# Optimization experiments

Hardware: AMD Instinct MI355X
Metric: run time of the kernel (lower is better)

The kernel has to match this reference:

```python
import jax, jax.numpy as jnp
import numpy as np

SEQ, BATCH, IN, HID, OUT = 512, 64, 512, 1024, 512
KEEP = 0.7  # dropout p = 0.3


def setup_inputs() -> dict:
    key = jax.random.key(0)
    ks = jax.random.split(key, 9)
    def lin(k, fan_out, fan_in):
        bound = 1.0 / np.sqrt(fan_in)
        kw, kb = jax.random.split(k)
        W = jax.random.uniform(kw, (fan_out, fan_in), jnp.float32, -bound, bound)
        b = jax.random.uniform(kb, (fan_out,), jnp.float32, -bound, bound)
        return W, b
    x = jax.random.normal(ks[0], (SEQ, BATCH, IN), jnp.float32)
    # inverted dropout mask, fixed for determinism
    drop_mask = (jax.random.bernoulli(ks[1], KEEP, (SEQ, BATCH, OUT))
                 .astype(jnp.float32) / KEEP)
    W_i2h, b_i2h = lin(ks[2], HID, IN + HID)
    W_i2o, b_i2o = lin(ks[3], OUT, IN + HID)
    W_o2o, b_o2o = lin(ks[4], OUT, HID + OUT)
    return {"x": x, "drop_mask": drop_mask,
            "W_i2h": W_i2h, "b_i2h": b_i2h,
            "W_i2o": W_i2o, "b_i2o": b_i2o,
            "W_o2o": W_o2o, "b_o2o": b_o2o}


def reference(x, drop_mask, W_i2h, b_i2h, W_i2o, b_i2o, W_o2o, b_o2o):
    # x: [S, B, IN]; returns log-probs [S, B, OUT]
    def step(h, inp):
        x_t, m_t = inp  # [B, IN], [B, OUT]
        comb = jnp.concatenate([x_t, h], axis=1)          # [B, IN+HID]
        out = comb @ W_i2o.T + b_i2o                      # [B, OUT]
        h_new = comb @ W_i2h.T + b_i2h                    # [B, HID]
        oc = jnp.concatenate([out, h_new], axis=1) @ W_o2o.T + b_o2o  # [B, OUT]
        oc = oc * m_t                                     # dropout (inverted mask)
        oc = jax.nn.log_softmax(oc, axis=-1)
        return h_new, oc
    h0 = jnp.zeros((x.shape[1], W_i2h.shape[0]), x.dtype)
    _, outs = jax.lax.scan(step, h0, (x, drop_mask))
    return outs
```

## Files before the change

kernel.cpp:

```cpp
#include <hip/hip_runtime.h>
#include <stdint.h>


typedef unsigned short ushort_t;
typedef __attribute__((ext_vector_type(8))) __bf16 bf16x8;
typedef __attribute__((ext_vector_type(4))) float f32x4;

__device__ __forceinline__ ushort_t f2bf(float f) {
  union { float f; uint32_t u; } v; v.f = f;
  uint32_t r = v.u + 0x7fffu + ((v.u >> 16) & 1u);
  return (ushort_t)(r >> 16);
}
__device__ __forceinline__ float bf2f(ushort_t b) {
  union { uint32_t u; float f; } v; v.u = ((uint32_t)b) << 16;
  return v.f;
}
__device__ __forceinline__ void gload16(const ushort_t* g, ushort_t* l) {
  __builtin_amdgcn_global_load_lds(
      (const __attribute__((address_space(1))) uint32_t*)g,
      (__attribute__((address_space(3))) uint32_t*)l, 16, 0, 0);
}

__global__ __launch_bounds__(256) void pack_kernel(
    const float* __restrict__ x, const float* __restrict__ mask,
    const float* __restrict__ W_i2h,
    const float* __restrict__ W_i2o, const float* __restrict__ W_o2o,
    const float* __restrict__ b_i2o, const float* __restrict__ b_o2o,
    ushort_t* xB, ushort_t* Wihx, ushort_t* Whh, ushort_t* Wiox,
    ushort_t* Wioh, ushort_t* Wo1, ushort_t* Wo2, float* biasP,
    uint64_t* maskb, uint32_t* harr0) {
  int64_t i = (int64_t)blockIdx.x * blockDim.x + threadIdx.x;
  const int64_t c0 = 16777216, c1 = 17301504, c2 = 18350080, c3 = 18612224,
                c4 = 19136512, c5 = 19398656, c6 = 19922944,
                cB = 19955712,
                cM = 36732928,
                cI = 36765696;
  if (i < c0) { xB[i] = f2bf(x[i]); return; }
  if (i < c1) { int64_t j = i - c0; int r = j >> 9,  c = j & 511;  Wihx[j] = f2bf(W_i2h[(int64_t)r * 1536 + c]); return; }
  if (i < c2) { int64_t j = i - c1; int r = j >> 10, c = j & 1023; Whh[j]  = f2bf(W_i2h[(int64_t)r * 1536 + 512 + c]); return; }
  if (i < c3) { int64_t j = i - c2; int r = j >> 9,  c = j & 511;  Wiox[j] = f2bf(W_i2o[(int64_t)r * 1536 + c]); return; }
  if (i < c4) { int64_t j = i - c3; int r = j >> 10, c = j & 1023; Wioh[j] = f2bf(W_i2o[(int64_t)r * 1536 + 512 + c]); return; }
  if (i < c5) { int64_t j = i - c4; int r = j >> 9,  c = j & 511;  Wo1[j]  = f2bf(W_o2o[(int64_t)r * 1536 + c]); return; }
  if (i < c6) { int64_t j = i - c5; int r = j >> 10, c = j & 1023; Wo2[j]  = f2bf(W_o2o[(int64_t)r * 1536 + 512 + c]); return; }
  if (i < cB) {
    int64_t q = i - c6;
    const int n = (int)(q >> 6), lane = (int)(q & 63);
    const float* wr = W_o2o + (int64_t)n * 1536;
    float s = 0.f;
#pragma unroll
    for (int k = 0; k < 8; ++k) {
      const int m = lane + 64 * k;
      s += wr[m] * b_i2o[m];
    }
#pragma unroll
    for (int off = 32; off; off >>= 1) s += __shfl_xor(s, off, 64);
    if (lane == 0) biasP[n] = s + b_o2o[n];
    return;
  }
  if (i < cM) {
    int64_t j = i - cB;
    float v = mask[j];
    uint64_t bits = __ballot(v != 0.0f);
    if ((j & 63) == 0) maskb[j >> 6] = bits;
    return;
  }
  if (i < cI) {
    harr0[i - cM] = 0;
  }
}

__device__ void usetup_tile(ushort_t* SH,
    const ushort_t* __restrict__ Wo1, const ushort_t* __restrict__ Wiox,
    const ushort_t* __restrict__ Wioh, ushort_t* __restrict__ U1,
    ushort_t* __restrict__ U2, int job) {
  ushort_t* AsF = SH;
  ushort_t* BsF = SH + 4096;
  const ushort_t* Bm; ushort_t* Om; int mt, nt, ldb;
  if (job < 16) { mt = job >> 2; nt = job & 3; Bm = Wiox; Om = U1; ldb = 512; }
  else { job -= 16; mt = job >> 3; nt = job & 7; Bm = Wioh; Om = U2; ldb = 1024; }
  const int m0 = mt * 128, n0 = nt * 128;
  const int tid = threadIdx.x;
  const int w = tid >> 6, l = tid & 63;
  const int quad = l >> 4, l15 = l & 15;
  const int wm = (w & 1) * 64, wn = (w >> 1) * 64;
  const int r0 = tid >> 2, chunk = tid & 3;
  f32x4 acc[4][4] = {};
  for (int k0 = 0; k0 < 512; k0 += 32) {
    __syncthreads();
    gload16(Wo1 + (size_t)(m0 + r0) * 512 + k0 + chunk * 8,      &AsF[tid * 8]);
    gload16(Wo1 + (size_t)(m0 + r0 + 64) * 512 + k0 + chunk * 8, &AsF[2048 + tid * 8]);
#pragma unroll
    for (int rep = 0; rep < 2; ++rep) {
      const int idx = tid + 256 * rep;
      const int kk = idx & 31, n8 = idx >> 5;
      union { uint4 v; ushort_t s[8]; } u;
      u.v = *(const uint4*)(Bm + (size_t)(k0 + kk) * ldb + n0 + n8 * 8);
#pragma unroll
      for (int i = 0; i < 8; ++i) BsF[(n8 * 8 + i) * 32 + kk] = u.s[i];
    }
    __syncthreads();
    bf16x8 af[4], bfr[4];
#pragma unroll
    for (int i = 0; i < 4; ++i) af[i]  = *(const bf16x8*)&AsF[(wm + 16 * i + l15) * 32 + 8 * quad];
#pragma unroll
    for (int j = 0; j < 4; ++j) bfr[j] = *(const bf16x8*)&BsF[(wn + 16 * j + l15) * 32 + 8 * quad];
#pragma unroll
    for (int i = 0; i < 4; ++i)
#pragma unroll
      for (int j = 0; j < 4; ++j)
        acc[i][j] = __builtin_amdgcn_mfma_f32_16x16x32_bf16(af[i], bfr[j], acc[i][j], 0, 0, 0);
  }
#pragma unroll
  for (int i = 0; i < 4; ++i) {
    const int row = m0 + wm + 16 * i + 4 * quad;
#pragma unroll
    for (int j = 0; j < 4; ++j) {
      const int col = n0 + wn + 16 * j + l15;
#pragma unroll
      for (int r = 0; r < 4; ++r)
        Om[(size_t)(row + r) * ldb + col] = f2bf(acc[i][j][r]);
    }
  }
}

__global__ __launch_bounds__(256) void gemm_bt(
    const ushort_t* __restrict__ A1, int lda1, const ushort_t* __restrict__ B1, int K1,
    const float* __restrict__ bias, ushort_t* Cb, int Ntiles,
    const ushort_t* __restrict__ Wo1, const ushort_t* __restrict__ Wiox,
    const ushort_t* __restrict__ Wioh, ushort_t* __restrict__ U1,
    ushort_t* __restrict__ U2) {
  __shared__ __align__(16) ushort_t SH[16384];
  if (blockIdx.x >= 2048) {
    usetup_tile(SH, Wo1, Wiox, Wioh, U1, U2, blockIdx.x - 2048);
    return;
  }
  const int mt = blockIdx.x & 255, nt = blockIdx.x >> 8;
  const int m0 = mt * 128, n0 = nt * 128;
  const int tid = threadIdx.x;
  const int w = tid >> 6, l = tid & 63;
  const int quad = l >> 4, l15 = l & 15;
  const int wm = (w & 1) * 64, wn = (w >> 1) * 64;
  const int r0 = tid >> 2, chunk = tid & 3;
  f32x4 acc[4][4] = {};
  gload16(A1 + (size_t)(m0 + r0) * lda1 + chunk * 8,      &SH[tid * 8]);
  gload16(A1 + (size_t)(m0 + r0 + 64) * lda1 + chunk * 8, &SH[2048 + tid * 8]);
  gload16(B1 + (size_t)(n0 + r0) * K1 + chunk * 8,        &SH[8192 + tid * 8]);
  gload16(B1 + (size_t)(n0 + r0 + 64) * K1 + chunk * 8,   &SH[8192 + 2048 + tid * 8]);
  const int NIT = K1 >> 5;
  for (int it = 0; it < NIT; ++it) {
    const int p = it & 1;
    const int ao = p * 4096, bo = 8192 + p * 4096;
    __syncthreads();
    if (it + 1 < NIT) {
      const int kn = (it + 1) * 32;
      const int an = (p ^ 1) * 4096, bn = 8192 + (p ^ 1) * 4096;
      gload16(A1 + (size_t)(m0 + r0) * lda1 + kn + chunk * 8,      &SH[an + tid * 8]);
      gload16(A1 + (size_t)(m0 + r0 + 64) * lda1 + kn + chunk * 8, &SH[an + 2048 + tid * 8]);
      gload16(B1 + (size_t)(n0 + r0) * K1 + kn + chunk * 8,        &SH[bn + tid * 8]);
      gload16(B1 + (size_t)(n0 + r0 + 64) * K1 + kn + chunk * 8,   &SH[bn + 2048 + tid * 8]);
    }
    bf16x8 af[4], bfr[4];
#pragma unroll
    for (int i = 0; i < 4; ++i) af[i]  = *(const bf16x8*)&SH[ao + (wm + 16 * i + l15) * 32 + 8 * quad];
#pragma unroll
    for (int j = 0; j < 4; ++j) bfr[j] = *(const bf16x8*)&SH[bo + (wn + 16 * j + l15) * 32 + 8 * quad];
#pragma unroll
    for (int i = 0; i < 4; ++i)
#pragma unroll
      for (int j = 0; j < 4; ++j)
        acc[i][j] = __builtin_amdgcn_mfma_f32_16x16x32_bf16(af[i], bfr[j], acc[i][j], 0, 0, 0);
  }
  const int N = Ntiles * 128;
#pragma unroll
  for (int i = 0; i < 4; ++i) {
    const int row = m0 + wm + 16 * i + 4 * quad;
#pragma unroll
    for (int j = 0; j < 4; ++j) {
      const int col = n0 + wn + 16 * j + l15;
      const float bv = bias[col];
#pragma unroll
      for (int r = 0; r < 4; ++r)
        Cb[(size_t)(row + r) * N + col] = f2bf(acc[i][j][r] + bv);
    }
  }
}

template<int NTERMS>
__device__ void pair_tile128T(ushort_t* SH,
    const ushort_t* __restrict__ A0r0, const ushort_t* __restrict__ A0r1,
    const ushort_t* __restrict__ B0,
    const ushort_t* __restrict__ A1r0, const ushort_t* __restrict__ A1r1,
    const ushort_t* __restrict__ B1,
    int n0, const ushort_t* __restrict__ Xh, ushort_t* __restrict__ Oh,
    int gate) {
  const int tid = threadIdx.x;
  const int w = tid >> 6, l = tid & 63;
  const int quad = l >> 4, l15 = l & 15;
  const int wm = (w & 1) * 64, wn = (w >> 1) * 64;
  const int r0 = tid >> 2, chunk = tid & 3;
  const int thrA  = r0 * 1024 + chunk * 8;
  const int thrB0 = (n0 + r0) * 1024 + chunk * 8;
  const int thrB1 = (n0 + r0 + 64) * 1024 + chunk * 8;
  const ushort_t* ga0 = A0r0 + thrA;
  const ushort_t* ga1 = A0r1 + thrA;
  const ushort_t* gb0 = B0 + thrB0;
  const ushort_t* gb1 = B0 + thrB1;
  f32x4 acc[4][4] = {};
  gload16(ga0, &SH[tid * 8]);
  gload16(ga1, &SH[2048 + tid * 8]);
  gload16(gb0, &SH[8192 + tid * 8]);
  gload16(gb1, &SH[8192 + 2048 + tid * 8]);
  const int NIT = NTERMS * 32;
  for (int it = 0; it < NIT; ++it) {
    const int p = it & 1;
    const int ap = p * 4096, bp = 8192 + p * 4096;
    __syncthreads();
    if (it + 1 < NIT) {
      if (NTERMS == 2 && it == 31) {
        ga0 = A1r0 + thrA; ga1 = A1r1 + thrA;
        gb0 = B1 + thrB0;  gb1 = B1 + thrB1;
      } else {
        ga0 += 32; ga1 += 32; gb0 += 32; gb1 += 32;
      }
      const int an = (p ^ 1) * 4096, bn = 8192 + (p ^ 1) * 4096;
      gload16(ga0, &SH[an + tid * 8]);
      gload16(ga1, &SH[an + 2048 + tid * 8]);
      gload16(gb0, &SH[bn + tid * 8]);
      gload16(gb1, &SH[bn + 2048 + tid * 8]);
    }
    bf16x8 af[4], bfr[4];
#pragma unroll
    for (int i = 0; i < 4; ++i) af[i]  = *(const bf16x8*)&SH[ap + (wm + 16 * i + l15) * 32 + 8 * quad];
#pragma unroll
    for (int j = 0; j < 4; ++j) bfr[j] = *(const bf16x8*)&SH[bp + (wn + 16 * j + l15) * 32 + 8 * quad];
#pragma unroll
    for (int i = 0; i < 4; ++i)
#pragma unroll
      for (int j = 0; j < 4; ++j)
        acc[i][j] = __builtin_amdgcn_mfma_f32_16x16x32_bf16(af[i], bfr[j], acc[i][j], 0, 0, 0);
  }
#pragma unroll
  for (int i = 0; i < 4; ++i) {
#pragma unroll
    for (int j = 0; j < 4; ++j) {
      const int col = n0 + wn + 16 * j + l15;
#pragma unroll
      for (int r = 0; r < 4; ++r) {
        const int lrow = 16 * i + 4 * quad + r;
        const size_t idx = (size_t)lrow * 1024 + col;
        float v = gate ? acc[i][j][r] : 0.0f;
        Oh[idx] = f2bf(v + bf2f(Xh[idx]));
      }
    }
  }
}

__device__ void copy_tile(const ushort_t* X, ushort_t* O, int n0) {
  const int t = threadIdx.x, r = t >> 2, q = t & 3;
  const uint4* src = (const uint4*)(X + (size_t)r * 1024 + n0 + q * 32);
  uint4* dst = (uint4*)(O + (size_t)r * 1024 + n0 + q * 32);
  dst[0] = src[0]; dst[1] = src[1]; dst[2] = src[2]; dst[3] = src[3];
}

__device__ void power_tile(ushort_t* SH,
                           const ushort_t* __restrict__ Am,
                           const ushort_t* __restrict__ Bm,
                           ushort_t* __restrict__ Om, int t) {
  ushort_t* AsF = SH;
  ushort_t* BsF = SH + 4096;
  const int mt = t & 7, nt = (t >> 3) & 7;
  const int m0 = mt * 128, n0 = nt * 128;
  const int tid = threadIdx.x;
  const int w = tid >> 6, l = tid & 63;
  const int quad = l >> 4, l15 = l & 15;
  const int wm = (w & 1) * 64, wn = (w >> 1) * 64;
  const int r0 = tid >> 2, chunk = tid & 3;
  f32x4 acc[4][4] = {};
  for (int k0 = 0; k0 < 1024; k0 += 32) {
    __syncthreads();
    gload16(Am + (size_t)(m0 + r0) * 1024 + k0 + chunk * 8,      &AsF[tid * 8]);
    gload16(Am + (size_t)(m0 + r0 + 64) * 1024 + k0 + chunk * 8, &AsF[2048 + tid * 8]);
#pragma unroll
    for (int rep = 0; rep < 2; ++rep) {
      const int idx = tid + 256 * rep;
      const int kk = idx & 31, n8 = idx >> 5;
      union { uint4 v; ushort_t s[8]; } u;
      u.v = *(const uint4*)(Bm + (size_t)(k0 + kk) * 1024 + n0 + n8 * 8);
#pragma unroll
      for (int i = 0; i < 8; ++i) BsF[(n8 * 8 + i) * 32 + kk] = u.s[i];
    }
    __syncthreads();
    bf16x8 af[4], bfr[4];
#pragma unroll
    for (int i = 0; i < 4; ++i) af[i]  = *(const bf16x8*)&AsF[(wm + 16 * i + l15) * 32 + 8 * quad];
#pragma unroll
    for (int j = 0; j < 4; ++j) bfr[j] = *(const bf16x8*)&BsF[(wn + 16 * j + l15) * 32 + 8 * quad];
#pragma unroll
    for (int i = 0; i < 4; ++i)
#pragma unroll
      for (int j = 0; j < 4; ++j)
        acc[i][j] = __builtin_amdgcn_mfma_f32_16x16x32_bf16(af[i], bfr[j], acc[i][j], 0, 0, 0);
  }
#pragma unroll
  for (int i = 0; i < 4; ++i) {
    const int row = m0 + wm + 16 * i + 4 * quad;
#pragma unroll
    for (int j = 0; j < 4; ++j) {
      const int col = n0 + wn + 16 * j + l15;
#pragma unroll
      for (int r = 0; r < 4; ++r)
        Om[(size_t)(row + r) * 1024 + col] = f2bf(acc[i][j][r]);
    }
  }
}

#define PWp(idx) (Pw + (size_t)(idx) * 1048576)

__global__ __launch_bounds__(256) void pass_kernel(
    const ushort_t* __restrict__ XhB, ushort_t* __restrict__ Harr,
    const ushort_t* __restrict__ Whh, ushort_t* __restrict__ Pw, int mode) {
  __shared__ __align__(16) ushort_t SH[16384];
  const int bid = blockIdx.x;
  const int npow = (mode == 1) ? 64 : ((mode == 2) ? 128 : 256);
  if (bid < npow) {
    const int pj = bid >> 6, t = bid & 63;
    const ushort_t *Am, *Bm; ushort_t* Om;
    if (mode == 1)      { Am = Whh;    Bm = Whh;    Om = PWp(0); }
    else if (mode == 2) {
      if (pj == 0) { Am = Whh;    Bm = PWp(0); Om = PWp(1); }
      else         { Am = PWp(0); Bm = PWp(0); Om = PWp(2); }
    } else {
      switch (pj) {
        case 0:  Am = Whh;    Bm = PWp(2); Om = PWp(3); break;
        case 1:  Am = PWp(0); Bm = PWp(2); Om = PWp(4); break;
        case 2:  Am = PWp(1); Bm = PWp(2); Om = PWp(5); break;
        default: Am = PWp(2); Bm = PWp(2); Om = PWp(6); break;
      }
    }
    power_tile(SH, Am, Bm, Om, t);
    return;
  }
  const int inner0 = bid - npow;
  const int u = inner0 >> 8, inner = inner0 & 255;
  const int p_ = (inner & 7) | (((inner >> 6) & 3) << 3);
  const int n0 = ((inner >> 3) & 7) * 128;
#define HS_(s) (Harr + (size_t)(s) * 65536)
#define XS_(s) (XhB + (size_t)(s) * 65536)
  const ushort_t *A0, *B0, *A1 = nullptr, *B1 = nullptr, *X; ushort_t* O;
  int terms = 1;
  if (mode == 1) {
    const int as[4] = {0, 2, 4, 6}, xs[4] = {1, 3, 5, 7}, os[4] = {2, 4, 1, 8};
    A0 = XS_(as[u]); B0 = Whh; X = XS_(xs[u]); O = HS_(os[u]);
  } else if (mode == 2) {
    if (u == 0)      { A0 = HS_(2); B0 = Whh;    X = XS_(2); O = HS_(3); }
    else if (u == 1) { A0 = HS_(2); B0 = PWp(0); X = HS_(4); O = HS_(4); }
    else             { A0 = HS_(1); B0 = PWp(0); X = HS_(8); O = HS_(8); }
  } else {
    if (u == 0)      { A0 = HS_(4); B0 = Whh;    X = XS_(4); O = HS_(5); }
    else if (u == 1) { A0 = HS_(4); B0 = PWp(0); X = HS_(1); O = HS_(6); }
    else if (u == 2) { A0 = HS_(1); B0 = Whh; A1 = HS_(4); B1 = PWp(1);
                       terms = 2;               X = XS_(6); O = HS_(7); }
    else             { A0 = HS_(4); B0 = PWp(2); X = HS_(8); O = HS_(8); }
  }
  const size_t co0 = (size_t)(2 * p_) * 524288;
  const size_t co1 = co0 + 524288;
  const int half = (threadIdx.x >> 6) & 1;
  const size_t coh = half ? co1 : co0;
  if (terms == 2)
    pair_tile128T<2>(SH, A0 + co0, A0 + co1, B0, A1 + co0, A1 + co1, B1,
                     n0, X + coh, O + coh, 1);
  else
    pair_tile128T<1>(SH, A0 + co0, A0 + co1, B0, nullptr, nullptr, nullptr,
                     n0, X + coh, O + coh, 1);
}

__global__ __launch_bounds__(256) void scan64(
    const ushort_t* __restrict__ old, ushort_t* __restrict__ nw,
    const ushort_t* __restrict__ Pv, int d,
    const ushort_t* __restrict__ Pra, ushort_t* __restrict__ Pwo, int nride) {
  __shared__ __align__(16) ushort_t SH[16384];
  if (blockIdx.x < nride) {
    power_tile(SH, Pra, Pra, Pwo, blockIdx.x);
    return;
  }
  const int bid = blockIdx.x - nride;
  const int p_ = (bid & 7) | (((bid >> 6) & 3) << 3);
  const int n0 = ((bid >> 3) & 7) * 128;
  const int c0 = 2 * p_, c1 = c0 + 1;
  if (c1 < d) {
    copy_tile(old + (size_t)c0 * 524288, nw + (size_t)c0 * 524288, n0);
    copy_tile(old + (size_t)c1 * 524288, nw + (size_t)c1 * 524288, n0);
    return;
  }
  const int ia0 = (c0 >= d) ? (c0 - d) : 0;
  const int ia1 = c1 - d;
  const int half = (threadIdx.x >> 6) & 1;
  const int ch = half ? c1 : c0;
  const int gate = (ch >= d);
  pair_tile128T<1>(SH, old + (size_t)ia0 * 524288, old + (size_t)ia1 * 524288,
                   Pv, nullptr, nullptr, nullptr, n0,
                   old + (size_t)ch * 524288, nw + (size_t)ch * 524288, gate);
}

__global__ __launch_bounds__(256) void correct_kernel(
    const ushort_t* __restrict__ S, const ushort_t* __restrict__ XhB,
    ushort_t* __restrict__ Harr, const ushort_t* __restrict__ Whh,
    const ushort_t* __restrict__ Pw) {
  __shared__ __align__(16) ushort_t AsF[2][4096];
  __shared__ __align__(16) ushort_t BsF[2][4096];
  const int p_ = blockIdx.x >> 3;
  const int n0 = (blockIdx.x & 7) * 128;
  const int j = blockIdx.y + 1;
  const ushort_t* Wj = (j == 1) ? Whh : (Pw + (size_t)(j - 2) * 1048576);
  const ushort_t* Xs = (j == 1) ? XhB : (Harr + (size_t)j * 65536);
  ushort_t* XO = Harr + (size_t)j * 65536;
  const int tid = threadIdx.x;
  const int w = tid >> 6, l = tid & 63;
  const int quad = l >> 4, l15 = l & 15;
  const int wm = (w & 1) * 64, wn = (w >> 1) * 64;
  const int r0 = tid >> 2, chunk = tid & 3;
  f32x4 acc[4][4] = {};
  const ushort_t* a0 = S + (size_t)(2 * p_) * 524288 + (size_t)r0 * 1024;
  const ushort_t* a1 = S + (size_t)(2 * p_ + 1) * 524288 + (size_t)r0 * 1024;
  gload16(a0 + chunk * 8, &AsF[0][tid * 8]);
  gload16(a1 + chunk * 8, &AsF[0][2048 + tid * 8]);
  gload16(Wj + (size_t)(n0 + r0) * 1024 + chunk * 8,      &BsF[0][tid * 8]);
  gload16(Wj + (size_t)(n0 + r0 + 64) * 1024 + chunk * 8, &BsF[0][2048 + tid * 8]);
  for (int it = 0; it < 32; ++it) {
    const int p = it & 1;
    __syncthreads();
    if (it < 31) {
      const int kn = (it + 1) * 32;
      gload16(a0 + kn + chunk * 8, &AsF[p ^ 1][tid * 8]);
      gload16(a1 + kn + chunk * 8, &AsF[p ^ 1][2048 + tid * 8]);
      gload16(Wj + (size_t)(n0 + r0) * 1024 + kn + chunk * 8,      &BsF[p ^ 1][tid * 8]);
      gload16(Wj + (size_t)(n0 + r0 + 64) * 1024 + kn + chunk * 8, &BsF[p ^ 1][2048 + tid * 8]);
    }
    bf16x8 af[4], bfr[4];
#pragma unroll
    for (int i = 0; i < 4; ++i) af[i]  = *(const bf16x8*)&AsF[p][(wm + 16 * i + l15) * 32 + 8 * quad];
#pragma unroll
    for (int jj = 0; jj < 4; ++jj) bfr[jj] = *(const bf16x8*)&BsF[p][(wn + 16 * jj + l15) * 32 + 8 * quad];
#pragma unroll
    for (int i = 0; i < 4; ++i)
#pragma unroll
      for (int jj = 0; jj < 4; ++jj)
        acc[i][jj] = __builtin_amdgcn_mfma_f32_16x16x32_bf16(af[i], bfr[jj], acc[i][jj], 0, 0, 0);
  }
#pragma unroll
  for (int i = 0; i < 4; ++i) {
#pragma unroll
    for (int jj = 0; jj < 4; ++jj) {
      const int col = n0 + wn + 16 * jj + l15;
#pragma unroll
      for (int r = 0; r < 4; ++r) {
        const int gr = wm + 16 * i + 4 * quad + r;
        const int c = 2 * p_ + (gr >> 6);
        const size_t idx = (size_t)c * 524288 + (size_t)(gr & 63) * 1024 + col;
        XO[idx] = f2bf(acc[i][jj][r] + bf2f(Xs[idx]));
      }
    }
  }
}

__global__ __launch_bounds__(256) void gemm_fused(
    const ushort_t* __restrict__ xB, const ushort_t* __restrict__ U1,
    const ushort_t* __restrict__ Harr, const ushort_t* __restrict__ U2,
    const ushort_t* __restrict__ Wo2, const float* __restrict__ biasP,
    const uint64_t* __restrict__ maskb, float* __restrict__ out) {
  __shared__ __align__(16) ushort_t AsF[2][4096];
  __shared__ __align__(16) ushort_t BsF[2][4096];
  const int mt = blockIdx.x & 255, nt = blockIdx.x >> 8;
  const int m0 = mt * 128, n0 = nt * 128;
  const int tid = threadIdx.x;
  const int w = tid >> 6, l = tid & 63;
  const int quad = l >> 4, l15 = l & 15;
  const int wm = (w & 1) * 64, wn = (w >> 1) * 64;
  const int r0 = tid >> 2, chunk = tid & 3;
  f32x4 acc[4][4] = {};
  auto issue = [&](int it, int b) {
    const ushort_t *A, *B; int K, k0;
    if (it < 16)      { A = xB;           B = U1;  K = 512;  k0 = it << 5; }
    else if (it < 48) { A = Harr;         B = U2;  K = 1024; k0 = (it - 16) << 5; }
    else              { A = Harr + 65536; B = Wo2; K = 1024; k0 = (it - 48) << 5; }
    gload16(A + (size_t)(m0 + r0) * K + k0 + chunk * 8,      &AsF[b][tid * 8]);
    gload16(A + (size_t)(m0 + r0 + 64) * K + k0 + chunk * 8, &AsF[b][2048 + tid * 8]);
    gload16(B + (size_t)(n0 + r0) * K + k0 + chunk * 8,      &BsF[b][tid * 8]);
    gload16(B + (size_t)(n0 + r0 + 64) * K + k0 + chunk * 8, &BsF[b][2048 + tid * 8]);
  };
  issue(0, 0);
  for (int it = 0; it < 80; ++it) {
    const int p = it & 1;
    __syncthreads();
    if (it < 79) issue(it + 1, p ^ 1);
    bf16x8 af[4], bfr[4];
#pragma unroll
    for (int i = 0; i < 4; ++i) af[i]  = *(const bf16x8*)&AsF[p][(wm + 16 * i + l15) * 32 + 8 * quad];
#pragma unroll
    for (int j = 0; j < 4; ++j) bfr[j] = *(const bf16x8*)&BsF[p][(wn + 16 * j + l15) * 32 + 8 * quad];
#pragma unroll
    for (int i = 0; i < 4; ++i)
#pragma unroll
      for (int j = 0; j < 4; ++j)
        acc[i][j] = __builtin_amdgcn_mfma_f32_16x16x32_bf16(af[i], bfr[j], acc[i][j], 0, 0, 0);
  }
  const float INV_KEEP = 1.0f / 0.7f;
#pragma unroll
  for (int i = 0; i < 4; ++i) {
    const int row = m0 + wm + 16 * i + 4 * quad;
#pragma unroll
    for (int j = 0; j < 4; ++j) {
      const int col = n0 + wn + 16 * j + l15;
      const float bv = biasP[col];
#pragma unroll
      for (int r = 0; r < 4; ++r) {
        const size_t idx = (size_t)(row + r) * 512 + col;
        const uint64_t bits = maskb[idx >> 6];
        out[idx] = ((bits >> (idx & 63)) & 1) ? (acc[i][j][r] + bv) * INV_KEEP
                                              : 0.0f;
      }
    }
  }
}

__global__ __launch_bounds__(256) void softmax_kernel(float* __restrict__ out) {
  const int row = blockIdx.x;
  const int tid = threadIdx.x;
  const size_t base = (size_t)row * 512;
  __shared__ float sm[4], ss[4];
  const float v0 = out[base + tid];
  const float v1 = out[base + tid + 256];
  float m = fmaxf(v0, v1);
#pragma unroll
  for (int off = 32; off; off >>= 1) m = fmaxf(m, __shfl_xor(m, off, 64));
  const int w = tid >> 6;
  if ((tid & 63) == 0) sm[w] = m;
  __syncthreads();
  m = fmaxf(fmaxf(sm[0], sm[1]), fmaxf(sm[2], sm[3]));
  float s = __expf(v0 - m) + __expf(v1 - m);
#pragma unroll
  for (int off = 32; off; off >>= 1) s += __shfl_xor(s, off, 64);
  if ((tid & 63) == 0) ss[w] = s;
  __syncthreads();
  s = ss[0] + ss[1] + ss[2] + ss[3];
  const float lg = logf(s);
  out[base + tid] = v0 - m - lg;
  out[base + tid + 256] = v1 - m - lg;
}

extern "C" void kernel_launch(void* const* d_in, const int* in_sizes, int n_in,
                              void* d_out, int out_size, void* d_ws, size_t ws_size,
                              hipStream_t stream) {
  const float* x     = (const float*)d_in[0];
  const float* mask  = (const float*)d_in[1];
  const float* W_i2h = (const float*)d_in[2];
  const float* b_i2h = (const float*)d_in[3];
  const float* W_i2o = (const float*)d_in[4];
  const float* b_i2o = (const float*)d_in[5];
  const float* W_o2o = (const float*)d_in[6];
  const float* b_o2o = (const float*)d_in[7];
  float* out = (float*)d_out;

  char* ws = (char*)d_ws;
  const size_t NEED = 207749120;
  if (ws_size < NEED) return;
  ushort_t* xB   = (ushort_t*)(ws + 0);
  ushort_t* XhB  = (ushort_t*)(ws + 33554432);
  ushort_t* SA   = XhB + 65536;
  ushort_t* SB   = XhB + 3 * 65536;
  ushort_t* Harr = (ushort_t*)(ws + 100663296);
  ushort_t* Pw   = (ushort_t*)(ws + 167903232);
  ushort_t* U1   = (ushort_t*)(ws + 193069056);
  ushort_t* U2   = (ushort_t*)(ws + 193593344);
  float* biasP   = (float*)(ws + 194641920);
  uint64_t* maskb = (uint64_t*)(ws + 195000320);
  ushort_t* Wihx = (ushort_t*)(ws + 201457664);
  ushort_t* Whh  = (ushort_t*)(ws + 202506240);
  ushort_t* Wiox = (ushort_t*)(ws + 204603392);
  ushort_t* Wioh = (ushort_t*)(ws + 205127680);
  ushort_t* Wo1  = (ushort_t*)(ws + 206176256);
  ushort_t* Wo2  = (ushort_t*)(ws + 206700544);

  hipLaunchKernelGGL(pack_kernel, dim3(143616), dim3(256), 0, stream,
                     x, mask, W_i2h, W_i2o, W_o2o, b_i2o, b_o2o,
                     xB, Wihx, Whh, Wiox, Wioh, Wo1, Wo2, biasP, maskb,
                     (uint32_t*)Harr);
  hipLaunchKernelGGL(gemm_bt, dim3(2096), dim3(256), 0, stream,
                     xB, 512, Wihx, 512, b_i2h, XhB, 8,
                     Wo1, Wiox, Wioh, U1, U2);
  hipLaunchKernelGGL(pass_kernel, dim3(1088), dim3(256), 0, stream,
                     XhB, Harr, Whh, Pw, 1);
  hipLaunchKernelGGL(pass_kernel, dim3(896), dim3(256), 0, stream,
                     XhB, Harr, Whh, Pw, 2);
  hipLaunchKernelGGL(pass_kernel, dim3(1280), dim3(256), 0, stream,
                     XhB, Harr, Whh, Pw, 3);
  hipLaunchKernelGGL(scan64, dim3(320), dim3(256), 0, stream, Harr, SB, PWp(6),  1, PWp(6),  PWp(7),  64);
  hipLaunchKernelGGL(scan64, dim3(320), dim3(256), 0, stream, SB, SA, PWp(7),  2, PWp(7),  PWp(8),  64);
  hipLaunchKernelGGL(scan64, dim3(320), dim3(256), 0, stream, SA, SB, PWp(8),  4, PWp(8),  PWp(9),  64);
  hipLaunchKernelGGL(scan64, dim3(320), dim3(256), 0, stream, SB, SA, PWp(9),  8, PWp(9),  PWp(10), 64);
  hipLaunchKernelGGL(scan64, dim3(320), dim3(256), 0, stream, SA, SB, PWp(10), 16, PWp(10), PWp(11), 64);
  hipLaunchKernelGGL(scan64, dim3(256), dim3(256), 0, stream, SB, SA, PWp(11), 32, (const ushort_t*)nullptr, (ushort_t*)nullptr, 0);
  hipLaunchKernelGGL(correct_kernel, dim3(dim3(256, 8)), dim3(256), 0, stream,
                     SA, XhB, Harr, Whh, Pw);
  hipLaunchKernelGGL(gemm_fused, dim3(1024), dim3(256), 0, stream,
                     xB, U1, Harr, U2, Wo2, biasP, maskb, out);
  hipLaunchKernelGGL(softmax_kernel, dim3(32768), dim3(256), 0, stream, out);
}
```

Baseline: 1.113 ms.

## Fold correction GEMM tiles into scan passes and use wave-per-row softmax

Correction tiles for chunk pairs whose scan prefix is already final are now computed inside the later scan64 launches as extra blocks, overlapping them with the remaining scan steps. The standalone correct_kernel then handles only the last 16 pairs. Softmax is rewritten so one wavefront owns a row, with vectorized float4 loads and no shared-memory barriers. This adds complexity around which scan buffer holds finalized prefixes at each step, and a wrong pair-to-step mapping would silently produce incorrect values.

```diff
diff --git a/kernel.cpp b/kernel.cpp
--- a/kernel.cpp
+++ b/kernel.cpp
@@ -316,6 +316,64 @@
 
 #define PWp(idx) (Pw + (size_t)(idx) * 1048576)
 
+__device__ void correct_ride(ushort_t* SH,
+    const ushort_t* __restrict__ S, const ushort_t* __restrict__ XhB,
+    ushort_t* __restrict__ Harr, const ushort_t* __restrict__ Whh,
+    const ushort_t* __restrict__ Pw, int p_, int n0, int j) {
+  const ushort_t* Wj = (j == 1) ? Whh : (Pw + (size_t)(j - 2) * 1048576);
+  const ushort_t* Xs = (j == 1) ? XhB : (Harr + (size_t)j * 65536);
+  ushort_t* XO = Harr + (size_t)j * 65536;
+  const int tid = threadIdx.x;
+  const int w = tid >> 6, l = tid & 63;
+  const int quad = l >> 4, l15 = l & 15;
+  const int wm = (w & 1) * 64, wn = (w >> 1) * 64;
+  const int r0 = tid >> 2, chunk = tid & 3;
+  f32x4 acc[4][4] = {};
+  const ushort_t* a0 = S + (size_t)(2 * p_) * 524288 + (size_t)r0 * 1024;
+  const ushort_t* a1 = S + (size_t)(2 * p_ + 1) * 524288 + (size_t)r0 * 1024;
+  gload16(a0 + chunk * 8, &SH[tid * 8]);
+  gload16(a1 + chunk * 8, &SH[2048 + tid * 8]);
+  gload16(Wj + (size_t)(n0 + r0) * 1024 + chunk * 8,      &SH[8192 + tid * 8]);
+  gload16(Wj + (size_t)(n0 + r0 + 64) * 1024 + chunk * 8, &SH[8192 + 2048 + tid * 8]);
+  for (int it = 0; it < 32; ++it) {
+    const int p = it & 1;
+    const int ap = p * 4096, bp = 8192 + p * 4096;
+    __syncthreads();
+    if (it < 31) {
+      const int kn = (it + 1) * 32;
+      const int an = (p ^ 1) * 4096, bn = 8192 + (p ^ 1) * 4096;
+      gload16(a0 + kn + chunk * 8, &SH[an + tid * 8]);
+      gload16(a1 + kn + chunk * 8, &SH[an + 2048 + tid * 8]);
+      gload16(Wj + (size_t)(n0 + r0) * 1024 + kn + chunk * 8,      &SH[bn + tid * 8]);
+      gload16(Wj + (size_t)(n0 + r0 + 64) * 1024 + kn + chunk * 8, &SH[bn + 2048 + tid * 8]);
+    }
+    bf16x8 af[4], bfr[4];
+#pragma unroll
+    for (int i = 0; i < 4; ++i) af[i]  = *(const bf16x8*)&SH[ap + (wm + 16 * i + l15) * 32 + 8 * quad];
+#pragma unroll
+    for (int jj = 0; jj < 4; ++jj) bfr[jj] = *(const bf16x8*)&SH[bp + (wn + 16 * jj + l15) * 32 + 8 * quad];
+#pragma unroll
+    for (int i = 0; i < 4; ++i)
+#pragma unroll
+      for (int jj = 0; jj < 4; ++jj)
+        acc[i][jj] = __builtin_amdgcn_mfma_f32_16x16x32_bf16(af[i], bfr[jj], acc[i][jj], 0, 0, 0);
+  }
+#pragma unroll
+  for (int i = 0; i < 4; ++i) {
+#pragma unroll
+    for (int jj = 0; jj < 4; ++jj) {
+      const int col = n0 + wn + 16 * jj + l15;
+#pragma unroll
+      for (int r = 0; r < 4; ++r) {
+        const int gr = wm + 16 * i + 4 * quad + r;
+        const int c = 2 * p_ + (gr >> 6);
+        const size_t idx = (size_t)c * 524288 + (size_t)(gr & 63) * 1024 + col;
+        XO[idx] = f2bf(acc[i][jj][r] + bf2f(Xs[idx]));
+      }
+    }
+  }
+}
+
 __global__ __launch_bounds__(256) void pass_kernel(
     const ushort_t* __restrict__ XhB, ushort_t* __restrict__ Harr,
     const ushort_t* __restrict__ Whh, ushort_t* __restrict__ Pw, int mode) {
@@ -377,10 +435,21 @@
 __global__ __launch_bounds__(256) void scan64(
     const ushort_t* __restrict__ old, ushort_t* __restrict__ nw,
     const ushort_t* __restrict__ Pv, int d,
-    const ushort_t* __restrict__ Pra, ushort_t* __restrict__ Pwo, int nride) {
+    const ushort_t* __restrict__ Pra, ushort_t* __restrict__ Pwo, int nride,
+    const ushort_t* __restrict__ XhB, ushort_t* __restrict__ Harr,
+    const ushort_t* __restrict__ Whh, const ushort_t* __restrict__ Pw,
+    int crBase, int ncr) {
   __shared__ __align__(16) ushort_t SH[16384];
   if (blockIdx.x < nride) {
     power_tile(SH, Pra, Pra, Pwo, blockIdx.x);
+    return;
+  }
+  if (blockIdx.x >= nride + 256) {
+    const int q = blockIdx.x - (nride + 256);
+    const int pair = crBase + (q >> 6);
+    const int r = q & 63;
+    correct_ride(SH, old, XhB, Harr, Whh, Pw, pair, (r & 7) * 128,
+                 (r >> 3) + 1);
     return;
   }
   const int bid = blockIdx.x - nride;
@@ -408,7 +477,7 @@
     const ushort_t* __restrict__ Pw) {
   __shared__ __align__(16) ushort_t AsF[2][4096];
   __shared__ __align__(16) ushort_t BsF[2][4096];
-  const int p_ = blockIdx.x >> 3;
+  const int p_ = 16 + (blockIdx.x >> 3);
   const int n0 = (blockIdx.x & 7) * 128;
   const int j = blockIdx.y + 1;
   const ushort_t* Wj = (j == 1) ? Whh : (Pw + (size_t)(j - 2) * 1048576);
@@ -524,28 +593,25 @@
 }
 
 __global__ __launch_bounds__(256) void softmax_kernel(float* __restrict__ out) {
-  const int row = blockIdx.x;
-  const int tid = threadIdx.x;
-  const size_t base = (size_t)row * 512;
-  __shared__ float sm[4], ss[4];
-  const float v0 = out[base + tid];
-  const float v1 = out[base + tid + 256];
-  float m = fmaxf(v0, v1);
+  const int row = blockIdx.x * 4 + (threadIdx.x >> 6);
+  const int lane = threadIdx.x & 63;
+  const size_t base = (size_t)row * 512 + (size_t)lane * 8;
+  float4 v0 = *(const float4*)&out[base];
+  float4 v1 = *(const float4*)&out[base + 4];
+  float m = fmaxf(fmaxf(fmaxf(v0.x, v0.y), fmaxf(v0.z, v0.w)),
+                  fmaxf(fmaxf(v1.x, v1.y), fmaxf(v1.z, v1.w)));
 #pragma unroll
   for (int off = 32; off; off >>= 1) m = fmaxf(m, __shfl_xor(m, off, 64));
-  const int w = tid >> 6;
-  if ((tid & 63) == 0) sm[w] = m;
-  __syncthreads();
-  m = fmaxf(fmaxf(sm[0], sm[1]), fmaxf(sm[2], sm[3]));
-  float s = __expf(v0 - m) + __expf(v1 - m);
+  float s = __expf(v0.x - m) + __expf(v0.y - m) + __expf(v0.z - m) +
+            __expf(v0.w - m) + __expf(v1.x - m) + __expf(v1.y - m) +
+            __expf(v1.z - m) + __expf(v1.w - m);
 #pragma unroll
   for (int off = 32; off; off >>= 1) s += __shfl_xor(s, off, 64);
-  if ((tid & 63) == 0) ss[w] = s;
-  __syncthreads();
-  s = ss[0] + ss[1] + ss[2] + ss[3];
-  const float lg = logf(s);
-  out[base + tid] = v0 - m - lg;
-  out[base + tid + 256] = v1 - m - lg;
+  const float sh = m + logf(s);
+  v0.x -= sh; v0.y -= sh; v0.z -= sh; v0.w -= sh;
+  v1.x -= sh; v1.y -= sh; v1.z -= sh; v1.w -= sh;
+  *(float4*)&out[base] = v0;
+  *(float4*)&out[base + 4] = v1;
 }
 
 extern "C" void kernel_launch(void* const* d_in, const int* in_sizes, int n_in,
@@ -594,15 +660,22 @@
                      XhB, Harr, Whh, Pw, 2);
   hipLaunchKernelGGL(pass_kernel, dim3(1280), dim3(256), 0, stream,
                      XhB, Harr, Whh, Pw, 3);
-  hipLaunchKernelGGL(scan64, dim3(320), dim3(256), 0, stream, Harr, SB, PWp(6),  1, PWp(6),  PWp(7),  64);
-  hipLaunchKernelGGL(scan64, dim3(320), dim3(256), 0, stream, SB, SA, PWp(7),  2, PWp(7),  PWp(8),  64);
-  hipLaunchKernelGGL(scan64, dim3(320), dim3(256), 0, stream, SA, SB, PWp(8),  4, PWp(8),  PWp(9),  64);
-  hipLaunchKernelGGL(scan64, dim3(320), dim3(256), 0, stream, SB, SA, PWp(9),  8, PWp(9),  PWp(10), 64);
-  hipLaunchKernelGGL(scan64, dim3(320), dim3(256), 0, stream, SA, SB, PWp(10), 16, PWp(10), PWp(11), 64);
-  hipLaunchKernelGGL(scan64, dim3(256), dim3(256), 0, stream, SB, SA, PWp(11), 32, (const ushort_t*)nullptr, (ushort_t*)nullptr, 0);
-  hipLaunchKernelGGL(correct_kernel, dim3(dim3(256, 8)), dim3(256), 0, stream,
+  hipLaunchKernelGGL(scan64, dim3(320), dim3(256), 0, stream, Harr, SB, PWp(6),  1, PWp(6),  PWp(7),  64,
+                     XhB, Harr, Whh, Pw, 0, 0);
+  hipLaunchKernelGGL(scan64, dim3(384), dim3(256), 0, stream, SB, SA, PWp(7),  2, PWp(7),  PWp(8),  64,
+                     XhB, Harr, Whh, Pw, 0, 1);
+  hipLaunchKernelGGL(scan64, dim3(384), dim3(256), 0, stream, SA, SB, PWp(8),  4, PWp(8),  PWp(9),  64,
+                     XhB, Harr, Whh, Pw, 1, 1);
+  hipLaunchKernelGGL(scan64, dim3(448), dim3(256), 0, stream, SB, SA, PWp(9),  8, PWp(9),  PWp(10), 64,
+                     XhB, Harr, Whh, Pw, 2, 2);
+  hipLaunchKernelGGL(scan64, dim3(576), dim3(256), 0, stream, SA, SB, PWp(10), 16, PWp(10), PWp(11), 64,
+                     XhB, Harr, Whh, Pw, 4, 4);
+  hipLaunchKernelGGL(scan64, dim3(768), dim3(256), 0, stream, SB, SA, PWp(11), 32,
+                     (const ushort_t*)nullptr, (ushort_t*)nullptr, 0,
+                     XhB, Harr, Whh, Pw, 8, 8);
+  hipLaunchKernelGGL(correct_kernel, dim3(dim3(128, 8)), dim3(256), 0, stream,
                      SA, XhB, Harr, Whh, Pw);
   hipLaunchKernelGGL(gemm_fused, dim3(1024), dim3(256), 0, stream,
                      xB, U1, Harr, U2, Wo2, biasP, maskb, out);
-  hipLaunchKernelGGL(softmax_kernel, dim3(32768), dim3(256), 0, stream, out);
-}
+  hipLaunchKernelGGL(softmax_kernel, dim3(8192), dim3(256), 0, stream, out);
+}
```

New measurement: 1.139 ms. 2.4% more time.
